# Optimization experiments

Hardware: AMD Instinct MI355X
Metric: run time of the kernel (lower is better)

Reference implementation:

```python
import jax, jax.numpy as jnp
import numpy as np

L, H, C, D, B, OUT = 3, 4, 128, 128, 64, 128  # layers, heads, out_ch per head, in_dim, graphs, out_dim
NEG_SLOPE = 0.2
EPS = 1e-5


def _layernorm(x, g, b):
    mu = x.mean(-1, keepdims=True)
    var = ((x - mu) ** 2).mean(-1, keepdims=True)
    return (x - mu) * jax.lax.rsqrt(var + EPS) * g + b


def setup_inputs() -> dict:
    key = jax.random.key(0)
    ks = jax.random.split(key, 20)
    N, E = 50000, 400000
    x = jax.random.normal(ks[0], (N, D), jnp.float32)
    edge_index = jax.random.randint(ks[1], (2, E), 0, N, jnp.int64)
    batch = jnp.sort(jax.random.randint(ks[2], (N,), 0, B, jnp.int64))
    s = 1.0 / np.sqrt(D)
    inp = dict(x=x, edge_index=edge_index, batch=batch)
    inp["Wl"] = jax.random.normal(ks[3], (L, H, C, D), jnp.float32) * s
    inp["bl"] = jnp.zeros((L, H, C), jnp.float32)
    inp["Wr"] = jax.random.normal(ks[4], (L, H, C, D), jnp.float32) * s
    inp["br"] = jnp.zeros((L, H, C), jnp.float32)
    inp["att"] = jax.random.normal(ks[5], (L, H, C), jnp.float32) * (1.0 / np.sqrt(C))
    inp["conv_bias"] = jnp.zeros((L, C), jnp.float32)
    inp["ln_gamma"] = jnp.ones((L, C), jnp.float32)
    inp["ln_beta"] = jnp.zeros((L, C), jnp.float32)
    inp["W1"] = jax.random.normal(ks[6], (2 * C, C), jnp.float32) * (1.0 / np.sqrt(C))
    inp["b1"] = jnp.zeros((2 * C,), jnp.float32)
    inp["W2"] = jax.random.normal(ks[7], (OUT, 2 * C), jnp.float32) * (1.0 / np.sqrt(2 * C))
    inp["b2"] = jnp.zeros((OUT,), jnp.float32)
    inp["og"] = jnp.ones((OUT,), jnp.float32)
    inp["ob"] = jnp.zeros((OUT,), jnp.float32)
    return inp


def reference(x, edge_index, batch, Wl, bl, Wr, br, att, conv_bias, ln_gamma, ln_beta, W1, b1, W2, b2, og, ob):
    N = x.shape[0]
    loops = jnp.arange(N, dtype=edge_index.dtype)
    src = jnp.concatenate([edge_index[0], loops])  # [E+N]
    dst = jnp.concatenate([edge_index[1], loops])
    h = x  # input_proj is Identity (node_feat_dim == hidden_dim)
    for l in range(L):
        xl = jnp.einsum('nd,hcd->nhc', h, Wl[l]) + bl[l]  # [N,H,C]
        xr = jnp.einsum('nd,hcd->nhc', h, Wr[l]) + br[l]
        e = jax.nn.leaky_relu(xl[src] + xr[dst], NEG_SLOPE)  # [E+N,H,C]
        logits = jnp.einsum('ehc,hc->eh', e, att[l])  # [E+N,H]
        m = jax.ops.segment_max(logits, dst, num_segments=N)  # [N,H]
        p = jnp.exp(logits - m[dst])
        denom = jax.ops.segment_sum(p, dst, num_segments=N)
        alpha = p / denom[dst]  # segment softmax (self loops guarantee denom>0)
        out = jax.ops.segment_sum(xl[src] * alpha[:, :, None], dst, num_segments=N)  # [N,H,C]
        out = out.mean(axis=1) + conv_bias[l]  # concat=False -> mean over heads
        out = jax.nn.relu(_layernorm(out, ln_gamma[l], ln_beta[l]))
        h = h + out  # residual
    # global mean pool
    sums = jax.ops.segment_sum(h, batch, num_segments=B)
    cnt = jax.ops.segment_sum(jnp.ones((N,), h.dtype), batch, num_segments=B)
    g = sums / jnp.maximum(cnt, 1.0)[:, None]
    # MLP head + out norm
    g = jax.nn.gelu(g @ W1.T + b1, approximate=False) @ W2.T + b2
    return _layernorm(g, og, ob)
```

## Files before the change

kernel.cpp:

```cpp
#include <hip/hip_runtime.h>
#include <hip/hip_bf16.h>

typedef __bf16 bf16x4 __attribute__((ext_vector_type(4)));
typedef float f32x4 __attribute__((ext_vector_type(4)));
typedef float f32x2 __attribute__((ext_vector_type(2)));
typedef unsigned char u8;
typedef unsigned long long u64;

#define EPS 1e-5f

static __device__ __forceinline__ int lower_bound_i(const int* __restrict__ arr, int n, int val) {
  int lo = 0, hi = n;
  while (lo < hi) { int mid = (lo + hi) >> 1; if (arr[mid] < val) lo = mid + 1; else hi = mid; }
  return lo;
}

template <int CTRL>
static __device__ __forceinline__ float dpp_add(float x) {
  int s = __builtin_amdgcn_mov_dpp(__float_as_int(x), CTRL, 0xF, 0xF, true);
  return x + __int_as_float(s);
}
static __device__ __forceinline__ float row16_reduce(float t) {
  t = dpp_add<0xB1>(t);
  t = dpp_add<0x4E>(t);
  t = dpp_add<0x141>(t);
  t = dpp_add<0x140>(t);
  return t;
}

static __device__ __forceinline__ u8 f32_to_fp8(float v) {
  int pk = __builtin_amdgcn_cvt_pk_fp8_f32(v, v, 0, false);
  return (u8)(pk & 0xFF);
}
static __device__ __forceinline__ unsigned pack4_fp8(float a, float b, float c, float d) {
  int w = __builtin_amdgcn_cvt_pk_fp8_f32(a, b, 0, false);
  w = __builtin_amdgcn_cvt_pk_fp8_f32(c, d, w, true);
  return (unsigned)w;
}

__global__ void detect_dtypes(const unsigned* __restrict__ xw, const unsigned* __restrict__ eiw,
                              int* __restrict__ flags) {
  __shared__ int s_bf16, s_i64nz;
  int t = threadIdx.x;
  if (t == 0) { s_bf16 = 0; s_i64nz = 0; }
  __syncthreads();
  unsigned w = xw[t * 97];
  unsigned lo = w & 0xFFFFu;
  unsigned e = (lo >> 7) & 0xFF;
  int looks_bf16 = (lo == 0u) || (e >= 0x6A && e <= 0x86);
  atomicAdd(&s_bf16, looks_bf16);
  int k = t * 1031;
  int nz = (eiw[2 * k + 1] != 0u) ? 1 : 0;
  atomicAdd(&s_i64nz, nz);
  __syncthreads();
  if (t == 0) {
    flags[0] = (s_bf16 >= 192) ? 1 : 0;
    flags[1] = (s_i64nz == 0) ? 1 : 0;
  }
}

__global__ void canon_x(const void* __restrict__ src, float* __restrict__ h_f32,
                        u8* __restrict__ h8, int n4, const int* __restrict__ flags) {
  int i = blockIdx.x * blockDim.x + threadIdx.x;
  if (i >= n4) return;
  float v0, v1, v2, v3;
  if (flags[0]) {
    bf16x4 u = ((const bf16x4*)src)[i];
    v0 = (float)u[0]; v1 = (float)u[1]; v2 = (float)u[2]; v3 = (float)u[3];
  } else {
    float4 u = ((const float4*)src)[i];
    v0 = u.x; v1 = u.y; v2 = u.z; v3 = u.w;
  }
  ((float4*)h_f32)[i] = make_float4(v0, v1, v2, v3);
  ((unsigned*)h8)[i] = pack4_fp8(v0, v1, v2, v3);
}

struct ParamDesc { const void* src[12]; int off[13]; };

__global__ void canon_params(ParamDesc pd, float* __restrict__ dst, const int* __restrict__ flags,
                             int total) {
  int i = blockIdx.x * blockDim.x + threadIdx.x;
  if (i >= total) return;
  int s = 0;
#pragma unroll
  for (int k = 1; k < 12; k++) if (i >= pd.off[k]) s = k;
  int j = i - pd.off[s];
  const void* sp = pd.src[s];
  dst[i] = flags[0] ? (float)((const __bf16*)sp)[j] : ((const float*)sp)[j];
}

__global__ void canon_w8(const void* __restrict__ s1, const void* __restrict__ s2,
                         u8* __restrict__ dst, int n, const int* __restrict__ flags) {
  int i = blockIdx.x * blockDim.x + threadIdx.x;
  if (i >= 2 * n) return;
  const void* sp = (i < n) ? s1 : s2;
  int j = (i < n) ? i : i - n;
  float v = flags[0] ? (float)((const __bf16*)sp)[j] : ((const float*)sp)[j];
  dst[i] = f32_to_fp8(v);
}

__global__ void canon_ints(const void* __restrict__ ei_src, const void* __restrict__ bat_src,
                           int* __restrict__ ei32, int* __restrict__ bat32,
                           int* __restrict__ deg, int E, int N, const int* __restrict__ flags) {
  int i = blockIdx.x * blockDim.x + threadIdx.x;
  int total = 2 * E + N;
  if (i >= total) return;
  int i64 = flags[1];
  if (i < 2 * E) {
    int v = i64 ? (int)((const long long*)ei_src)[i] : ((const int*)ei_src)[i];
    ei32[i] = v;
    if (i >= E) atomicAdd(&deg[v], 1);
  } else {
    int j = i - 2 * E;
    int v = i64 ? (int)((const long long*)bat_src)[j] : ((const int*)bat_src)[j];
    bat32[j] = v;
    atomicAdd(&deg[j], 1);
  }
}

__global__ __launch_bounds__(256) void block_sums(const int* __restrict__ deg,
                                                  int* __restrict__ bsum, int N) {
  __shared__ int sh[256];
  int i = blockIdx.x * 256 + threadIdx.x;
  int t = threadIdx.x;
  sh[t] = (i < N) ? deg[i] : 0;
  __syncthreads();
  for (int off = 128; off > 0; off >>= 1) {
    if (t < off) sh[t] += sh[t + off];
    __syncthreads();
  }
  if (t == 0) bsum[blockIdx.x] = sh[0];
}

__global__ __launch_bounds__(256) void scan_bsums(const int* __restrict__ bsum,
                                                  int* __restrict__ bpref, int nblocks,
                                                  int* __restrict__ offs, int N) {
  __shared__ int sh[256];
  int t = threadIdx.x;
  int carry = 0;
  for (int base = 0; base < nblocks; base += 256) {
    int idx = base + t;
    int v = (idx < nblocks) ? bsum[idx] : 0;
    sh[t] = v;
    __syncthreads();
    for (int off = 1; off < 256; off <<= 1) {
      int u = (t >= off) ? sh[t - off] : 0;
      __syncthreads();
      sh[t] += u;
      __syncthreads();
    }
    if (idx < nblocks) bpref[idx] = carry + sh[t] - v;
    carry += sh[255];
    __syncthreads();
  }
  if (t == 0) offs[N] = carry;
}

__global__ __launch_bounds__(256) void write_offs(const int* __restrict__ deg,
                                                  const int* __restrict__ bpref,
                                                  int* __restrict__ offs,
                                                  int* __restrict__ cursor, int N) {
  __shared__ int sh[256];
  int i = blockIdx.x * 256 + threadIdx.x;
  int t = threadIdx.x;
  int v = (i < N) ? deg[i] : 0;
  sh[t] = v;
  __syncthreads();
  for (int off = 1; off < 256; off <<= 1) {
    int u = (t >= off) ? sh[t - off] : 0;
    __syncthreads();
    sh[t] += u;
    __syncthreads();
  }
  if (i < N) {
    int ex = bpref[blockIdx.x] + sh[t] - v;
    offs[i] = ex;
    cursor[i] = ex;
  }
}

__global__ void fill_csr(const int* __restrict__ ei, int E, int N,
                         int* __restrict__ cursor, int* __restrict__ csr_src) {
  int e = blockIdx.x * blockDim.x + threadIdx.x;
  if (e >= E + N) return;
  int s, d;
  if (e < E) { s = ei[e]; d = ei[E + e]; } else { s = e - E; d = e - E; }
  int pos = atomicAdd(&cursor[d], 1);
  csr_src[pos] = s * 1024;
}

__global__ __launch_bounds__(256) void gemm_xlr(
    const u8* __restrict__ A8, const u8* __restrict__ Wl8,
    const u8* __restrict__ Wr8, const float* __restrict__ bl,
    const float* __restrict__ br, u8* __restrict__ out8, int Nrows) {
  __shared__ u64 As[128][19];
  __shared__ u64 Ws[128][19];
  const int jb = blockIdx.y;
  const u8* Wbase = (jb < 4) ? (Wl8 + (size_t)jb * 16384) : (Wr8 + (size_t)(jb - 4) * 16384);
  const float* biasbase = (jb < 4) ? (bl + jb * 128) : (br + (jb - 4) * 128);
  const int row0 = blockIdx.x * 128;
  const int tid = threadIdx.x;
  const int lane = tid & 63, wave = tid >> 6;
  const int wm = wave >> 1, wn = wave & 1;

#pragma unroll
  for (int p = 0; p < 4; p++) {
    int r = (tid >> 3) + p * 32;
    int qc = (tid & 7) * 2;
    int gr = row0 + r;
    uint4 av = make_uint4(0, 0, 0, 0);
    if (gr < Nrows) av = *(const uint4*)(A8 + (size_t)gr * 128 + qc * 8);
    As[r][qc]     = ((u64)av.y << 32) | av.x;
    As[r][qc + 1] = ((u64)av.w << 32) | av.z;
    uint4 wv = *(const uint4*)(Wbase + (size_t)r * 128 + qc * 8);
    Ws[r][qc]     = ((u64)wv.y << 32) | wv.x;
    Ws[r][qc + 1] = ((u64)wv.w << 32) | wv.z;
  }
  __syncthreads();

  f32x4 acc[4][4];
#pragma unroll
  for (int mi = 0; mi < 4; mi++)
#pragma unroll
    for (int ni = 0; ni < 4; ni++) acc[mi][ni] = f32x4{0.f, 0.f, 0.f, 0.f};

#pragma unroll
  for (int ks = 0; ks < 4; ks++) {
    int qk = ks * 4 + (lane >> 4);
    long af[4], bf[4];
#pragma unroll
    for (int i = 0; i < 4; i++) {
      af[i] = (long)As[wm * 64 + i * 16 + (lane & 15)][qk];
      bf[i] = (long)Ws[wn * 64 + i * 16 + (lane & 15)][qk];
    }
#pragma unroll
    for (int mi = 0; mi < 4; mi++)
#pragma unroll
      for (int ni = 0; ni < 4; ni++)
        acc[mi][ni] = __builtin_amdgcn_mfma_f32_16x16x32_fp8_fp8(bf[ni], af[mi], acc[mi][ni], 0, 0, 0);
  }

#pragma unroll
  for (int mi = 0; mi < 4; mi++) {
    int gr = row0 + wm * 64 + mi * 16 + (lane & 15);
    if (gr >= Nrows) continue;
#pragma unroll
    for (int ni = 0; ni < 4; ni++) {
      int col_base = wn * 64 + ni * 16 + (lane >> 4) * 4;
      float4 b4 = *(const float4*)(biasbase + col_base);
      unsigned pk = pack4_fp8(acc[mi][ni][0] + b4.x, acc[mi][ni][1] + b4.y,
                              acc[mi][ni][2] + b4.z, acc[mi][ni][3] + b4.w);
      *(unsigned*)(out8 + (size_t)gr * 1024 + jb * 128 + col_base) = pk;
    }
  }
}

__global__ __launch_bounds__(256) void gat_fused(
    const u8* __restrict__ comb8, const float* __restrict__ att,
    const int* __restrict__ offs, const int* __restrict__ csr_src,
    const float* __restrict__ conv_bias, const float* __restrict__ gamma,
    const float* __restrict__ beta, float* __restrict__ h_f32,
    u8* __restrict__ h8, int N, int store_fp8) {
  int wid = blockIdx.x * 4 + (threadIdx.x >> 6);
  int lane = threadIdx.x & 63;
  if (wid >= N) return;
  int n = wid;
  f32x2 xr2[4], at2[4];
  uint2 wr = *(const uint2*)(comb8 + (size_t)n * 1024 + 512 + lane * 8);
  xr2[0] = __builtin_amdgcn_cvt_pk_f32_fp8(wr.x, false);
  xr2[1] = __builtin_amdgcn_cvt_pk_f32_fp8(wr.x, true);
  xr2[2] = __builtin_amdgcn_cvt_pk_f32_fp8(wr.y, false);
  xr2[3] = __builtin_amdgcn_cvt_pk_f32_fp8(wr.y, true);
  float4 a0 = *(const float4*)(att + lane * 8);
  float4 a1 = *(const float4*)(att + lane * 8 + 4);
  at2[0] = f32x2{a0.x, a0.y}; at2[1] = f32x2{a0.z, a0.w};
  at2[2] = f32x2{a1.x, a1.y}; at2[3] = f32x2{a1.z, a1.w};

  int off0 = offs[n], off1 = offs[n + 1];
  float l = 0.f;
  f32x2 acc2[4];
#pragma unroll
  for (int j = 0; j < 4; j++) acc2[j] = f32x2{0.f, 0.f};

  const u8* lane_base = comb8 + lane * 8;

  auto process = [&](uint2 w) {
    f32x2 x2[4];
    x2[0] = __builtin_amdgcn_cvt_pk_f32_fp8(w.x, false);
    x2[1] = __builtin_amdgcn_cvt_pk_f32_fp8(w.x, true);
    x2[2] = __builtin_amdgcn_cvt_pk_f32_fp8(w.y, false);
    x2[3] = __builtin_amdgcn_cvt_pk_f32_fp8(w.y, true);
    f32x2 t2 = f32x2{0.f, 0.f};
#pragma unroll
    for (int j = 0; j < 4; j++) {
      f32x2 z = x2[j] + xr2[j];
      f32x2 lz = __builtin_elementwise_max(z, 0.2f * z);
      t2 = t2 + lz * at2[j];
    }
    float t = t2[0] + t2[1];
    t = row16_reduce(t);
    t = fminf(fmaxf(t, -60.f), 60.f);
    float p = __expf(t);
    l += p;
    f32x2 p2 = f32x2{p, p};
#pragma unroll
    for (int j = 0; j < 4; j++) acc2[j] = acc2[j] + p2 * x2[j];
  };

  int pos = off0;
  for (; pos + 2 <= off1; pos += 2) {
    int b0 = csr_src[pos], b1 = csr_src[pos + 1];
    uint2 wa = *(const uint2*)(lane_base + (size_t)(unsigned)b0);
    uint2 wb = *(const uint2*)(lane_base + (size_t)(unsigned)b1);
    process(wa);
    process(wb);
  }
  if (pos < off1) {
    int b0 = csr_src[pos];
    uint2 wa = *(const uint2*)(lane_base + (size_t)(unsigned)b0);
    process(wa);
  }

  float invl = 1.0f / fmaxf(l, 1e-30f);
  float acc[8];
#pragma unroll
  for (int j = 0; j < 4; j++) {
    acc[2 * j]     = acc2[j][0] * invl;
    acc[2 * j + 1] = acc2[j][1] * invl;
  }
#pragma unroll
  for (int j = 0; j < 8; j++) {
    acc[j] += __shfl_xor(acc[j], 16);
    acc[j] += __shfl_xor(acc[j], 32);
  }
  int c0 = (lane & 15) * 8;
  float v[8];
  float s = 0.f, s2 = 0.f;
#pragma unroll
  for (int j = 0; j < 8; j++) {
    v[j] = acc[j] * 0.25f + conv_bias[c0 + j];
    s += v[j]; s2 += v[j] * v[j];
  }
  s = row16_reduce(s);
  s2 = row16_reduce(s2);
  float mu = s * (1.f / 128.f);
  float var = fmaxf(s2 * (1.f / 128.f) - mu * mu, 0.f);
  float rs = rsqrtf(var + EPS);
  if (lane < 16) {
    float4 o0, o1;
    float hn[8];
#pragma unroll
    for (int j = 0; j < 8; j++) {
      float o = (v[j] - mu) * rs * gamma[c0 + j] + beta[c0 + j];
      o = o > 0.f ? o : 0.f;
      hn[j] = h_f32[(size_t)n * 128 + c0 + j] + o;
    }
    o0.x = hn[0]; o0.y = hn[1]; o0.z = hn[2]; o0.w = hn[3];
    o1.x = hn[4]; o1.y = hn[5]; o1.z = hn[6]; o1.w = hn[7];
    *(float4*)(h_f32 + (size_t)n * 128 + c0) = o0;
    *(float4*)(h_f32 + (size_t)n * 128 + c0 + 4) = o1;
    if (store_fp8) {
      uint2 pk;
      pk.x = pack4_fp8(hn[0], hn[1], hn[2], hn[3]);
      pk.y = pack4_fp8(hn[4], hn[5], hn[6], hn[7]);
      *(uint2*)(h8 + (size_t)n * 128 + c0) = pk;
    }
  }
}

__global__ __launch_bounds__(128) void pool(const float* __restrict__ h_f32,
                                            const int* __restrict__ batch, int N,
                                            float* __restrict__ g_sum) {
  int g = blockIdx.x >> 4, slice = blockIdx.x & 15;
  int c = threadIdx.x;
  int r0 = lower_bound_i(batch, N, g);
  int r1 = lower_bound_i(batch, N, g + 1);
  int len = r1 - r0;
  if (len <= 0) return;
  int per = (len + 15) / 16;
  int s0 = r0 + slice * per;
  int s1 = min(s0 + per, r1);
  if (s0 >= s1) return;
  float acc = 0.f;
  for (int r = s0; r < s1; r++) acc += h_f32[(size_t)r * 128 + c];
  atomicAdd(&g_sum[g * 128 + c], acc);
}

__global__ __launch_bounds__(256) void mlp_head(
    const float* __restrict__ g_sum, const int* __restrict__ batch, int N,
    const float* __restrict__ W1, const float* __restrict__ b1,
    const float* __restrict__ W2, const float* __restrict__ b2,
    const float* __restrict__ og, const float* __restrict__ ob,
    void* __restrict__ outv, const int* __restrict__ flags) {
  __shared__ float gld[128];
  __shared__ float hid[256];
  __shared__ float olds[128];
  __shared__ float red[2];
  int b = blockIdx.x, t = threadIdx.x;
  int r0 = lower_bound_i(batch, N, b);
  int r1 = lower_bound_i(batch, N, b + 1);
  int len = r1 - r0;
  float cntf = (float)(len < 1 ? 1 : len);
  if (t < 128) gld[t] = g_sum[b * 128 + t] / cntf;
  __syncthreads();
  float sacc = b1[t];
  for (int d = 0; d < 128; d++) sacc = fmaf(gld[d], W1[(size_t)t * 128 + d], sacc);
  hid[t] = 0.5f * sacc * (1.f + erff(sacc * 0.70710678118654752f));
  __syncthreads();
  if (t < 128) {
    float o = b2[t];
    for (int k = 0; k < 256; k++) o = fmaf(hid[k], W2[(size_t)t * 256 + k], o);
    olds[t] = o;
  }
  __syncthreads();
  if (t < 64) {
    float a = olds[t], bb = olds[t + 64];
    float s = a + bb, s2 = a * a + bb * bb;
    for (int off = 32; off; off >>= 1) { s += __shfl_down(s, off); s2 += __shfl_down(s2, off); }
    if (t == 0) { red[0] = s * (1.f / 128.f); red[1] = s2 * (1.f / 128.f); }
  }
  __syncthreads();
  if (t < 128) {
    float mu = red[0];
    float var = fmaxf(red[1] - mu * mu, 0.f);
    float rs = rsqrtf(var + EPS);
    float o = (olds[t] - mu) * rs * og[t] + ob[t];
    if (flags[0]) ((__bf16*)outv)[b * 128 + t] = (__bf16)o;
    else          ((float*)outv)[b * 128 + t] = o;
  }
}

extern "C" void kernel_launch(void* const* d_in, const int* in_sizes, int n_in,
                              void* d_out, int out_size, void* d_ws, size_t ws_size,
                              hipStream_t stream) {
  const int D = 128, B = 64;
  const int N = in_sizes[0] / D;
  const int E = in_sizes[1] / 2;
  const int EN = E + N;
  const int nsb = (N + 255) / 256;

  char* p = (char*)d_ws;
  auto alloc = [&](size_t bytes) {
    char* r = p; p += (bytes + 255) & ~(size_t)255; return (void*)r;
  };
  int* flags     = (int*)alloc(256);
  float* h_f32   = (float*)alloc((size_t)N * 128 * 4);
  u8* h8         = (u8*)alloc((size_t)N * 128);
  u8* comb8      = (u8*)alloc((size_t)N * 1024);
  int* deg       = (int*)alloc((size_t)N * 4);
  int* offs      = (int*)alloc((size_t)(N + 1) * 4);
  int* cursor    = (int*)alloc((size_t)N * 4);
  int* csr_src   = (int*)alloc((size_t)EN * 4);
  float* g_sum   = (float*)alloc((size_t)B * 128 * 4);
  int* ei32      = (int*)alloc((size_t)2 * E * 4);
  int* bat32     = (int*)alloc((size_t)N * 4);
  int* bsum      = (int*)alloc((size_t)nsb * 4);
  int* bpref     = (int*)alloc((size_t)nsb * 4);
  u8* w8         = (u8*)alloc((size_t)2 * 196608);
  float* params  = (float*)alloc((size_t)71936 * 4);

  float* bl_c  = params + 0;
  float* br_c  = params + 1536;
  float* att_c = params + 3072;
  float* cb_c  = params + 4608;
  float* g_c   = params + 4992;
  float* b_c   = params + 5376;
  float* W1_c  = params + 5760;
  float* b1_c  = params + 38528;
  float* W2_c  = params + 38784;
  float* b2_c  = params + 71552;
  float* og_c  = params + 71680;
  float* ob_c  = params + 71808;

  detect_dtypes<<<1, 256, 0, stream>>>((const unsigned*)d_in[0], (const unsigned*)d_in[1], flags);

  canon_x<<<(N * 32 + 255) / 256, 256, 0, stream>>>(d_in[0], h_f32, h8, N * 32, flags);

  ParamDesc pd;
  const int srcidx[12] = {4, 6, 7, 8, 9, 10, 11, 12, 13, 14, 15, 16};
  const int sizes12[12] = {1536, 1536, 1536, 384, 384, 384, 32768, 256, 32768, 128, 128, 128};
  int cum = 0;
  for (int k = 0; k < 12; k++) { pd.src[k] = d_in[srcidx[k]]; pd.off[k] = cum; cum += sizes12[k]; }
  pd.off[12] = cum;
  canon_params<<<(cum + 255) / 256, 256, 0, stream>>>(pd, params, flags, cum);

  canon_w8<<<(2 * 196608 + 255) / 256, 256, 0, stream>>>(d_in[3], d_in[5], w8, 196608, flags);

  hipMemsetAsync(deg, 0, (size_t)N * 4, stream);
  hipMemsetAsync(g_sum, 0, (size_t)B * 128 * 4, stream);

  canon_ints<<<(2 * E + N + 255) / 256, 256, 0, stream>>>(d_in[1], d_in[2], ei32, bat32, deg, E, N, flags);
  block_sums<<<nsb, 256, 0, stream>>>(deg, bsum, N);
  scan_bsums<<<1, 256, 0, stream>>>(bsum, bpref, nsb, offs, N);
  write_offs<<<nsb, 256, 0, stream>>>(deg, bpref, offs, cursor, N);
  fill_csr<<<(EN + 255) / 256, 256, 0, stream>>>(ei32, E, N, cursor, csr_src);

  for (int l = 0; l < 3; l++) {
    gemm_xlr<<<dim3((N + 127) / 128, 8), 256, 0, stream>>>(
        h8, w8 + (size_t)l * 65536, w8 + 196608 + (size_t)l * 65536,
        bl_c + l * 512, br_c + l * 512, comb8, N);
    gat_fused<<<(N + 3) / 4, 256, 0, stream>>>(comb8, att_c + l * 512, offs, csr_src,
        cb_c + l * 128, g_c + l * 128, b_c + l * 128, h_f32, h8, N, (l < 2) ? 1 : 0);
  }
  pool<<<B * 16, 128, 0, stream>>>(h_f32, bat32, N, g_sum);
  mlp_head<<<B, 256, 0, stream>>>(g_sum, bat32, N, W1_c, b1_c, W2_c, b2_c, og_c, ob_c, d_out, flags);
}
```

Before: 522.8 us.

## Fuse canonicalization kernels and process GAT nodes in degree-sorted order

Result: slower. 687.9 us (+31.6%).

```diff
diff --git a/kernel.cpp b/kernel.cpp
--- a/kernel.cpp
+++ b/kernel.cpp
@@ -59,44 +59,45 @@
   }
 }
 
-__global__ void canon_x(const void* __restrict__ src, float* __restrict__ h_f32,
-                        u8* __restrict__ h8, int n4, const int* __restrict__ flags) {
+struct ParamDesc { const void* src[12]; int off[13]; };
+
+__global__ void canon_all(const void* __restrict__ xsrc, ParamDesc pd,
+                          const void* __restrict__ w1, const void* __restrict__ w2,
+                          float* __restrict__ h_f32, u8* __restrict__ h8,
+                          float* __restrict__ params, u8* __restrict__ w8,
+                          int n_x4, int n_par, int n_w, const int* __restrict__ flags) {
   int i = blockIdx.x * blockDim.x + threadIdx.x;
-  if (i >= n4) return;
-  float v0, v1, v2, v3;
-  if (flags[0]) {
-    bf16x4 u = ((const bf16x4*)src)[i];
-    v0 = (float)u[0]; v1 = (float)u[1]; v2 = (float)u[2]; v3 = (float)u[3];
-  } else {
-    float4 u = ((const float4*)src)[i];
-    v0 = u.x; v1 = u.y; v2 = u.z; v3 = u.w;
-  }
-  ((float4*)h_f32)[i] = make_float4(v0, v1, v2, v3);
-  ((unsigned*)h8)[i] = pack4_fp8(v0, v1, v2, v3);
-}
-
-struct ParamDesc { const void* src[12]; int off[13]; };
-
-__global__ void canon_params(ParamDesc pd, float* __restrict__ dst, const int* __restrict__ flags,
-                             int total) {
-  int i = blockIdx.x * blockDim.x + threadIdx.x;
-  if (i >= total) return;
-  int s = 0;
-#pragma unroll
-  for (int k = 1; k < 12; k++) if (i >= pd.off[k]) s = k;
-  int j = i - pd.off[s];
-  const void* sp = pd.src[s];
-  dst[i] = flags[0] ? (float)((const __bf16*)sp)[j] : ((const float*)sp)[j];
-}
-
-__global__ void canon_w8(const void* __restrict__ s1, const void* __restrict__ s2,
-                         u8* __restrict__ dst, int n, const int* __restrict__ flags) {
-  int i = blockIdx.x * blockDim.x + threadIdx.x;
-  if (i >= 2 * n) return;
-  const void* sp = (i < n) ? s1 : s2;
-  int j = (i < n) ? i : i - n;
-  float v = flags[0] ? (float)((const __bf16*)sp)[j] : ((const float*)sp)[j];
-  dst[i] = f32_to_fp8(v);
+  int isbf = flags[0];
+  if (i < n_x4) {
+    float v0, v1, v2, v3;
+    if (isbf) {
+      bf16x4 u = ((const bf16x4*)xsrc)[i];
+      v0 = (float)u[0]; v1 = (float)u[1]; v2 = (float)u[2]; v3 = (float)u[3];
+    } else {
+      float4 u = ((const float4*)xsrc)[i];
+      v0 = u.x; v1 = u.y; v2 = u.z; v3 = u.w;
+    }
+    ((float4*)h_f32)[i] = make_float4(v0, v1, v2, v3);
+    ((unsigned*)h8)[i] = pack4_fp8(v0, v1, v2, v3);
+    return;
+  }
+  i -= n_x4;
+  if (i < n_par) {
+    int s = 0;
+#pragma unroll
+    for (int k = 1; k < 12; k++) if (i >= pd.off[k]) s = k;
+    int j = i - pd.off[s];
+    const void* sp = pd.src[s];
+    params[i] = isbf ? (float)((const __bf16*)sp)[j] : ((const float*)sp)[j];
+    return;
+  }
+  i -= n_par;
+  if (i < 2 * n_w) {
+    const void* sp = (i < n_w) ? w1 : w2;
+    int j = (i < n_w) ? i : i - n_w;
+    float v = isbf ? (float)((const __bf16*)sp)[j] : ((const float*)sp)[j];
+    w8[i] = f32_to_fp8(v);
+  }
 }
 
 __global__ void canon_ints(const void* __restrict__ ei_src, const void* __restrict__ bat_src,
@@ -119,22 +120,30 @@
 }
 
 __global__ __launch_bounds__(256) void block_sums(const int* __restrict__ deg,
-                                                  int* __restrict__ bsum, int N) {
+                                                  int* __restrict__ bsum,
+                                                  int* __restrict__ hist, int N) {
   __shared__ int sh[256];
+  __shared__ int lh[64];
   int i = blockIdx.x * 256 + threadIdx.x;
   int t = threadIdx.x;
-  sh[t] = (i < N) ? deg[i] : 0;
-  __syncthreads();
+  int v = (i < N) ? deg[i] : 0;
+  sh[t] = v;
+  if (t < 64) lh[t] = 0;
+  __syncthreads();
+  if (i < N) atomicAdd(&lh[min(v, 63)], 1);
   for (int off = 128; off > 0; off >>= 1) {
     if (t < off) sh[t] += sh[t + off];
     __syncthreads();
   }
   if (t == 0) bsum[blockIdx.x] = sh[0];
+  if (t < 64 && lh[t]) atomicAdd(&hist[t], lh[t]);
 }
 
 __global__ __launch_bounds__(256) void scan_bsums(const int* __restrict__ bsum,
                                                   int* __restrict__ bpref, int nblocks,
-                                                  int* __restrict__ offs, int N) {
+                                                  int* __restrict__ offs, int N,
+                                                  const int* __restrict__ hist,
+                                                  int* __restrict__ bcur) {
   __shared__ int sh[256];
   int t = threadIdx.x;
   int carry = 0;
@@ -154,12 +163,24 @@
     __syncthreads();
   }
   if (t == 0) offs[N] = carry;
+  __syncthreads();
+  if (t < 64) sh[t] = hist[t];
+  __syncthreads();
+  for (int off = 1; off < 64; off <<= 1) {
+    int u = (t >= off && t < 64) ? sh[t - off] : 0;
+    __syncthreads();
+    if (t < 64) sh[t] += u;
+    __syncthreads();
+  }
+  if (t < 64) bcur[t] = (t == 0) ? 0 : sh[t - 1];
 }
 
 __global__ __launch_bounds__(256) void write_offs(const int* __restrict__ deg,
                                                   const int* __restrict__ bpref,
                                                   int* __restrict__ offs,
-                                                  int* __restrict__ cursor, int N) {
+                                                  int* __restrict__ cursor,
+                                                  int* __restrict__ bcur,
+                                                  int* __restrict__ perm, int N) {
   __shared__ int sh[256];
   int i = blockIdx.x * 256 + threadIdx.x;
   int t = threadIdx.x;
@@ -176,6 +197,8 @@
     int ex = bpref[blockIdx.x] + sh[t] - v;
     offs[i] = ex;
     cursor[i] = ex;
+    int pos = atomicAdd(&bcur[min(v, 63)], 1);
+    perm[pos] = i;
   }
 }
 
@@ -258,13 +281,14 @@
 __global__ __launch_bounds__(256) void gat_fused(
     const u8* __restrict__ comb8, const float* __restrict__ att,
     const int* __restrict__ offs, const int* __restrict__ csr_src,
+    const int* __restrict__ perm,
     const float* __restrict__ conv_bias, const float* __restrict__ gamma,
     const float* __restrict__ beta, float* __restrict__ h_f32,
     u8* __restrict__ h8, int N, int store_fp8) {
   int wid = blockIdx.x * 4 + (threadIdx.x >> 6);
   int lane = threadIdx.x & 63;
   if (wid >= N) return;
-  int n = wid;
+  int n = perm[wid];
   f32x2 xr2[4], at2[4];
   uint2 wr = *(const uint2*)(comb8 + (size_t)n * 1024 + 512 + lane * 8);
   xr2[0] = __builtin_amdgcn_cvt_pk_f32_fp8(wr.x, false);
@@ -448,8 +472,11 @@
   u8* h8         = (u8*)alloc((size_t)N * 128);
   u8* comb8      = (u8*)alloc((size_t)N * 1024);
   int* deg       = (int*)alloc((size_t)N * 4);
+  int* hist      = (int*)alloc(256);
+  int* bcur      = (int*)alloc(256);
   int* offs      = (int*)alloc((size_t)(N + 1) * 4);
   int* cursor    = (int*)alloc((size_t)N * 4);
+  int* perm      = (int*)alloc((size_t)N * 4);
   int* csr_src   = (int*)alloc((size_t)EN * 4);
   float* g_sum   = (float*)alloc((size_t)B * 128 * 4);
   int* ei32      = (int*)alloc((size_t)2 * E * 4);
@@ -474,32 +501,34 @@
 
   detect_dtypes<<<1, 256, 0, stream>>>((const unsigned*)d_in[0], (const unsigned*)d_in[1], flags);
 
-  canon_x<<<(N * 32 + 255) / 256, 256, 0, stream>>>(d_in[0], h_f32, h8, N * 32, flags);
-
   ParamDesc pd;
   const int srcidx[12] = {4, 6, 7, 8, 9, 10, 11, 12, 13, 14, 15, 16};
   const int sizes12[12] = {1536, 1536, 1536, 384, 384, 384, 32768, 256, 32768, 128, 128, 128};
   int cum = 0;
   for (int k = 0; k < 12; k++) { pd.src[k] = d_in[srcidx[k]]; pd.off[k] = cum; cum += sizes12[k]; }
   pd.off[12] = cum;
-  canon_params<<<(cum + 255) / 256, 256, 0, stream>>>(pd, params, flags, cum);
-
-  canon_w8<<<(2 * 196608 + 255) / 256, 256, 0, stream>>>(d_in[3], d_in[5], w8, 196608, flags);
-
-  hipMemsetAsync(deg, 0, (size_t)N * 4, stream);
+
+  const int n_x4 = N * 32;
+  const int n_w = 196608;
+  const int canon_total = n_x4 + cum + 2 * n_w;
+  canon_all<<<(canon_total + 255) / 256, 256, 0, stream>>>(
+      d_in[0], pd, d_in[3], d_in[5], h_f32, h8, params, w8, n_x4, cum, n_w, flags);
+
+  size_t degR = ((size_t)N * 4 + 255) & ~(size_t)255;
+  hipMemsetAsync(deg, 0, degR + 512, stream);
   hipMemsetAsync(g_sum, 0, (size_t)B * 128 * 4, stream);
 
   canon_ints<<<(2 * E + N + 255) / 256, 256, 0, stream>>>(d_in[1], d_in[2], ei32, bat32, deg, E, N, flags);
-  block_sums<<<nsb, 256, 0, stream>>>(deg, bsum, N);
-  scan_bsums<<<1, 256, 0, stream>>>(bsum, bpref, nsb, offs, N);
-  write_offs<<<nsb, 256, 0, stream>>>(deg, bpref, offs, cursor, N);
+  block_sums<<<nsb, 256, 0, stream>>>(deg, bsum, hist, N);
+  scan_bsums<<<1, 256, 0, stream>>>(bsum, bpref, nsb, offs, N, hist, bcur);
+  write_offs<<<nsb, 256, 0, stream>>>(deg, bpref, offs, cursor, bcur, perm, N);
   fill_csr<<<(EN + 255) / 256, 256, 0, stream>>>(ei32, E, N, cursor, csr_src);
 
   for (int l = 0; l < 3; l++) {
     gemm_xlr<<<dim3((N + 127) / 128, 8), 256, 0, stream>>>(
         h8, w8 + (size_t)l * 65536, w8 + 196608 + (size_t)l * 65536,
         bl_c + l * 512, br_c + l * 512, comb8, N);
-    gat_fused<<<(N + 3) / 4, 256, 0, stream>>>(comb8, att_c + l * 512, offs, csr_src,
+    gat_fused<<<(N + 3) / 4, 256, 0, stream>>>(comb8, att_c + l * 512, offs, csr_src, perm,
         cb_c + l * 128, g_c + l * 128, b_c + l * 128, h_f32, h8, N, (l < 2) ? 1 : 0);
   }
   pool<<<B * 16, 128, 0, stream>>>(h_f32, bat32, N, g_sum);
```
